# Kernel optimization log

Measured on AMD Instinct MI355X. Metric: run time of the kernel, lower is better.

Reference implementation:

```python
import jax, jax.numpy as jnp
import numpy as np

D = 1024      # input_dim
H = 1024      # expert_hidden_dim
O = 1024      # output_dim
E = 8         # num_experts
TOPK = 2
B, N_OBJ = 4, 4096


def setup_inputs() -> dict:
    key = jax.random.key(0)
    ks = jax.random.split(key, 7)
    s_in = 1.0 / np.sqrt(D)
    s_h = 1.0 / np.sqrt(H)
    return {
        "x":  jax.random.normal(ks[0], (B, N_OBJ, D), dtype=jnp.float32),
        "Wr": jax.random.uniform(ks[1], (D, E), jnp.float32, -s_in, s_in),
        "br": jax.random.uniform(ks[2], (E,), jnp.float32, -s_in, s_in),
        "W1": jax.random.uniform(ks[3], (E, D, H), jnp.float32, -s_in, s_in),
        "b1": jax.random.uniform(ks[4], (E, H), jnp.float32, -s_in, s_in),
        "W2": jax.random.uniform(ks[5], (E, H, O), jnp.float32, -s_h, s_h),
        "b2": jax.random.uniform(ks[6], (E, O), jnp.float32, -s_h, s_h),
    }


def reference(x, Wr, br, W1, b1, W2, b2):
    # Router: (B, N, E)
    logits = jnp.einsum("bnd,de->bne", x, Wr) + br
    # sparse top-k routing: softmax over the top-k logits only
    topv, topi = jax.lax.top_k(logits, TOPK)          # (B, N, k)
    coef = jax.nn.softmax(topv, axis=-1)              # (B, N, k)
    # scatter per-expert coefficients into dense (B, N, E); zeros for non-selected
    coef_full = jnp.sum(
        jax.nn.one_hot(topi, E, dtype=x.dtype) * coef[..., None], axis=-2
    )                                                 # (B, N, E)
    # All-expert dense compute (as in original module; dropout is eval-mode identity)
    h = jax.nn.relu(jnp.einsum("bnd,edh->benh", x, W1) + b1[:, None, :])  # (B,E,N,H)
    y = jnp.einsum("benh,eho->beno", h, W2) + b2[:, None, :]              # (B,E,N,O)
    # Weighted combine over experts
    out = jnp.einsum("beno,bne->bno", y, coef_full)                        # (B,N,O)
    return out
```

## Files before the change

### kernel.cpp

```cpp
#include <hip/hip_runtime.h>
#include <cstdint>

typedef unsigned short u16;
using bf16x8 = __attribute__((ext_vector_type(8))) __bf16;
using f32x4  = __attribute__((ext_vector_type(4))) float;

#define T_TOK 16384
#define E_NUM 8

__device__ __forceinline__ u16 f2bf(float f) {
    union { float f; unsigned u; } v; v.f = f;
    unsigned r = (v.u + 0x7FFFu + ((v.u >> 16) & 1u)) >> 16;
    return (u16)r;
}

__device__ __forceinline__ void gload_lds16(const void* g, void* l) {
    __builtin_amdgcn_global_load_lds(
        (const __attribute__((address_space(1))) void*)g,
        (__attribute__((address_space(3))) void*)l, 16, 0, 0);
}

__global__ __launch_bounds__(256) void k_transpose(const float* __restrict__ W, u16* __restrict__ WT) {
    __shared__ float tile[32][33];
    int e = blockIdx.z;
    int d0 = blockIdx.x << 5, h0 = blockIdx.y << 5;
    int tx = threadIdx.x & 31, ty = threadIdx.x >> 5;
    const size_t eo = (size_t)e << 20;
#pragma unroll
    for (int i = 0; i < 4; ++i) {
        int r = ty + i * 8;
        tile[r][tx] = W[eo + (size_t)(d0 + r) * 1024 + h0 + tx];
    }
    __syncthreads();
#pragma unroll
    for (int i = 0; i < 4; ++i) {
        int r = ty + i * 8;
        WT[eo + (size_t)(h0 + r) * 1024 + d0 + tx] = f2bf(tile[tx][r]);
    }
}

__global__ __launch_bounds__(256) void k_router(const float* __restrict__ x, const float* __restrict__ Wr,
                                                const float* __restrict__ br,
                                                int* __restrict__ tinfo, float* __restrict__ c1arr,
                                                u16* __restrict__ xbf) {
    const int wave = threadIdx.x >> 6, lane = threadIdx.x & 63;
    const int t = (blockIdx.x << 2) + wave;
    const float* xr = x + (size_t)t * 1024;
    u16* xbr = xbf + (size_t)t * 1024;
    float acc[8] = {0, 0, 0, 0, 0, 0, 0, 0};
#pragma unroll
    for (int i = 0; i < 16; ++i) {
        int d = (i << 6) + lane;
        float xv = xr[d];
        xbr[d] = f2bf(xv);
        float4 w0 = *(const float4*)(Wr + d * 8);
        float4 w1 = *(const float4*)(Wr + d * 8 + 4);
        acc[0] += xv * w0.x; acc[1] += xv * w0.y; acc[2] += xv * w0.z; acc[3] += xv * w0.w;
        acc[4] += xv * w1.x; acc[5] += xv * w1.y; acc[6] += xv * w1.z; acc[7] += xv * w1.w;
    }
#pragma unroll
    for (int off = 32; off > 0; off >>= 1)
#pragma unroll
        for (int e = 0; e < 8; ++e) acc[e] += __shfl_xor(acc[e], off);

    if (lane == 0) {
        float v1 = -1e30f, v2 = -1e30f; int i1 = 0, i2 = 0;
#pragma unroll
        for (int e = 0; e < 8; ++e) {
            float v = acc[e] + br[e];
            if (v > v1) { v2 = v1; i2 = i1; v1 = v; i1 = e; }
            else if (v > v2) { v2 = v; i2 = e; }
        }
        float c1 = 1.f / (1.f + expf(v2 - v1));
        tinfo[t] = i1 | (i2 << 4);
        c1arr[t] = c1;
    }
}

__global__ __launch_bounds__(1024) void k_scatter(const int* __restrict__ tinfo, const float* __restrict__ c1arr,
                                                  int* __restrict__ cnt, int* __restrict__ tok,
                                                  float* __restrict__ coef) {
    __shared__ int lcnt[8];
    __shared__ int lbase[8];
    const int tid = threadIdx.x;
    const int t = blockIdx.x * 1024 + tid;
    if (tid < 8) lcnt[tid] = 0;
    __syncthreads();
    int info = tinfo[t];
    float c1 = c1arr[t];
    int g1 = info & 15;
    int g2 = (info >> 4) & 15;
    int o1 = atomicAdd(&lcnt[g1], 1);
    int o2 = atomicAdd(&lcnt[g2], 1);
    __syncthreads();
    if (tid < 8) lbase[tid] = atomicAdd(cnt + tid, lcnt[tid]);
    __syncthreads();
    int p1 = lbase[g1] + o1;
    tok[(g1 << 14) + p1] = t; coef[(g1 << 14) + p1] = c1;
    int p2 = lbase[g2] + o2;
    tok[(g2 << 14) + p2] = t; coef[(g2 << 14) + p2] = 1.f - c1;
}

template <int PHASE>
__global__ __launch_bounds__(256, 3) void k_gemm(
    const int* __restrict__ cnt, const int* __restrict__ tok, const float* __restrict__ coef,
    const u16* __restrict__ xbf, const u16* __restrict__ w1t, const u16* __restrict__ w2t,
    const float* __restrict__ b1, const float* __restrict__ b2,
    u16* __restrict__ hbuf, float* __restrict__ out)
{
    __shared__ u16 a0_s[128 * 64];
    __shared__ u16 a1_s[128 * 64];
    __shared__ u16 b0_s[64 * 64];
    __shared__ u16 b1_s[64 * 64];
    __shared__ int s_cnt[8];
    __shared__ int tok_s[128];
    __shared__ float coef_s[128];

    const int tid = threadIdx.x;
    if (tid < 8) s_cnt[tid] = cnt[tid];
    __syncthreads();

    int bid = blockIdx.x + blockIdx.y * 272;
    int lin = (bid & 7) * 544 + (bid >> 3);
    int xt = lin >> 4, yt = lin & 15;

    int g = -1, tile = 0, r0 = 0, mt = xt, rb = 0;
    for (int gg = 0; gg < 8; ++gg) {
        int c = s_cnt[gg], tg = (c + 127) >> 7;
        if (g < 0) {
            if (mt < tg) { g = gg; tile = mt; r0 = rb + (mt << 7); }
            else mt -= tg;
        }
        rb += c;
    }
    if (g < 0) return;
    const int cntg = s_cnt[g];
    const int e = g;
    const int nb = yt << 6;
    const int rowlim = cntg - (tile << 7);

    if (tid < 128) {
        int idx = (tile << 7) + tid;
        bool valid = idx < cntg;
        tok_s[tid] = valid ? tok[(g << 14) + idx] : 0;
        coef_s[tid] = valid ? coef[(g << 14) + idx] : 0.f;
    }
    __syncthreads();

    const int w = tid >> 6, l = tid & 63;
    const int wrow = (w >> 1) << 6, wcol = (w & 1) << 5;
    const u16* asrc = (PHASE == 0) ? xbf : hbuf;
    const u16* bsrc = (PHASE == 0) ? w1t : w2t;
    const size_t brow0 = ((size_t)e << 10) + nb;

    const int sw = ((l & 7) ^ (l >> 3)) << 3;
    const int xk = (l & 7) << 3;

    const u16* aptr[4]; int ldsa[4];
#pragma unroll
    for (int j = 0; j < 4; ++j) {
        int row = (j << 5) + (w << 3) + (l >> 3);
        int arow = (PHASE == 0) ? tok_s[row] : (r0 + row);
        aptr[j] = asrc + ((size_t)arow << 10) + sw;
        ldsa[j] = ((j << 5) + (w << 3)) * 64;
    }
    const u16* bptr[2]; int ldsb[2];
#pragma unroll
    for (int j = 0; j < 2; ++j) {
        int brow = (j << 5) + (w << 3) + (l >> 3);
        bptr[j] = bsrc + (brow0 + brow) * 1024 + sw;
        ldsb[j] = ((j << 5) + (w << 3)) * 64;
    }

    f32x4 acc[4][2];
#pragma unroll
    for (int mi = 0; mi < 4; ++mi)
#pragma unroll
        for (int ni = 0; ni < 2; ++ni) { acc[mi][ni][0] = 0.f; acc[mi][ni][1] = 0.f; acc[mi][ni][2] = 0.f; acc[mi][ni][3] = 0.f; }

#define STAGE(AS, BS, KO)                                                      \
    {                                                                          \
        _Pragma("unroll")                                                      \
        for (int j = 0; j < 4; ++j) gload_lds16(aptr[j] + (KO), &AS[ldsa[j]]); \
        _Pragma("unroll")                                                      \
        for (int j = 0; j < 2; ++j) gload_lds16(bptr[j] + (KO), &BS[ldsb[j]]); \
    }

#define COMPUTE(AS, BS)                                                        \
    {                                                                          \
        _Pragma("unroll")                                                      \
        for (int ks = 0; ks < 64; ks += 32) {                                  \
            const int co = (ks + ((l >> 4) << 3)) ^ xk;                        \
            bf16x8 af[4], bfr[2];                                              \
            _Pragma("unroll")                                                  \
            for (int mi = 0; mi < 4; ++mi)                                     \
                af[mi] = *(const bf16x8*)&AS[(wrow + (mi << 4) + (l & 15)) * 64 + co]; \
            _Pragma("unroll")                                                  \
            for (int ni = 0; ni < 2; ++ni)                                     \
                bfr[ni] = *(const bf16x8*)&BS[(wcol + (ni << 4) + (l & 15)) * 64 + co]; \
            _Pragma("unroll")                                                  \
            for (int mi = 0; mi < 4; ++mi)                                     \
                _Pragma("unroll")                                              \
                for (int ni = 0; ni < 2; ++ni)                                 \
                    acc[mi][ni] = __builtin_amdgcn_mfma_f32_16x16x32_bf16(af[mi], bfr[ni], acc[mi][ni], 0, 0, 0); \
        }                                                                      \
    }

#define VM6  asm volatile("s_waitcnt vmcnt(6)" ::: "memory")
#define VM0  asm volatile("s_waitcnt vmcnt(0)" ::: "memory")
#define LGK0 asm volatile("s_waitcnt lgkmcnt(0)" ::: "memory")
#define BAR() { asm volatile("" ::: "memory"); __builtin_amdgcn_s_barrier(); asm volatile("" ::: "memory"); }

    STAGE(a0_s, b0_s, 0);
    STAGE(a1_s, b1_s, 64);
    VM6; BAR();

    for (int kc = 0; kc < 12; kc += 2) {
        COMPUTE(a0_s, b0_s);
        LGK0; BAR();
        STAGE(a0_s, b0_s, (kc + 2) << 6);
        VM6; BAR();
        COMPUTE(a1_s, b1_s);
        LGK0; BAR();
        STAGE(a1_s, b1_s, (kc + 3) << 6);
        VM6; BAR();
    }
    COMPUTE(a0_s, b0_s);
    LGK0; BAR();
    STAGE(a0_s, b0_s, 14 << 6);
    VM6; BAR();
    COMPUTE(a1_s, b1_s);
    LGK0; BAR();
    STAGE(a1_s, b1_s, 15 << 6);
    VM6; BAR();
    COMPUTE(a0_s, b0_s);
    LGK0; BAR();
    VM0; BAR();
    COMPUTE(a1_s, b1_s);

#undef STAGE
#undef COMPUTE
#undef VM6
#undef VM0
#undef LGK0
#undef BAR

    const int rq = (l >> 4) << 2;
    const int cl = l & 15;
#pragma unroll
    for (int ni = 0; ni < 2; ++ni) {
        int ccol = wcol + (ni << 4) + cl;
        float bias = (PHASE == 0 ? b1 : b2)[((size_t)e << 10) + nb + ccol];
#pragma unroll
        for (int mi = 0; mi < 4; ++mi) {
            int rbase = wrow + (mi << 4) + rq;
#pragma unroll
            for (int j = 0; j < 4; ++j) {
                int r = rbase + j;
                if (r < rowlim) {
                    float v = acc[mi][ni][j] + bias;
                    if constexpr (PHASE == 0) {
                        v = fmaxf(v, 0.f);
                        hbuf[(size_t)(r0 + r) * 1024 + nb + ccol] = f2bf(v);
                    } else {
                        atomicAdd(out + ((size_t)tok_s[r] << 10) + nb + ccol, v * coef_s[r]);
                    }
                }
            }
        }
    }
}

__global__ __launch_bounds__(256) void k_naive(const float* __restrict__ x, const float* __restrict__ Wr,
    const float* __restrict__ br, const float* __restrict__ W1, const float* __restrict__ b1,
    const float* __restrict__ W2, const float* __restrict__ b2, float* __restrict__ out)
{
    __shared__ float xs[1024];
    __shared__ float hs[1024];
    __shared__ float red[4];
    __shared__ float lg[8];
    const int tid = threadIdx.x;
    const size_t t = blockIdx.x;
    for (int i = tid; i < 1024; i += 256) xs[i] = x[t * 1024 + i];
    __syncthreads();
    float lacc[8] = {0, 0, 0, 0, 0, 0, 0, 0};
    for (int d = tid; d < 1024; d += 256) {
        float xv = xs[d];
#pragma unroll
        for (int e = 0; e < 8; ++e) lacc[e] += xv * Wr[d * 8 + e];
    }
    for (int e = 0; e < 8; ++e) {
        float v = lacc[e];
        for (int off = 32; off > 0; off >>= 1) v += __shfl_xor(v, off);
        if ((tid & 63) == 0) red[tid >> 6] = v;
        __syncthreads();
        if (tid == 0) lg[e] = red[0] + red[1] + red[2] + red[3] + br[e];
        __syncthreads();
    }
    float v1 = -1e30f, v2 = -1e30f; int i1 = 0, i2 = 0;
    for (int e = 0; e < 8; ++e) {
        float v = lg[e];
        if (v > v1) { v2 = v1; i2 = i1; v1 = v; i1 = e; }
        else if (v > v2) { v2 = v; i2 = e; }
    }
    float c1 = 1.f / (1.f + expf(v2 - v1)), c2 = 1.f - c1;
    float yacc[4] = {0, 0, 0, 0};
    for (int slot = 0; slot < 2; ++slot) {
        int e = slot ? i2 : i1;
        float cw = slot ? c2 : c1;
        __syncthreads();
        float ha[4];
        for (int jb = 0; jb < 4; ++jb) {
            int j = (jb << 8) + tid;
            float a = b1[(e << 10) + j];
            for (int d = 0; d < 1024; ++d) a += xs[d] * W1[(((size_t)e << 10) + d) * 1024 + j];
            ha[jb] = fmaxf(a, 0.f);
        }
        for (int jb = 0; jb < 4; ++jb) hs[(jb << 8) + tid] = ha[jb];
        __syncthreads();
        for (int ob = 0; ob < 4; ++ob) {
            int o = (ob << 8) + tid;
            float a = b2[(e << 10) + o];
            for (int h = 0; h < 1024; ++h) a += hs[h] * W2[(((size_t)e << 10) + h) * 1024 + o];
            yacc[ob] += cw * a;
        }
    }
    for (int ob = 0; ob < 4; ++ob) out[t * 1024 + (ob << 8) + tid] = yacc[ob];
}

extern "C" void kernel_launch(void* const* d_in, const int* in_sizes, int n_in,
                              void* d_out, int out_size, void* d_ws, size_t ws_size,
                              hipStream_t stream) {
    const float* x  = (const float*)d_in[0];
    const float* Wr = (const float*)d_in[1];
    const float* br = (const float*)d_in[2];
    const float* W1 = (const float*)d_in[3];
    const float* b1 = (const float*)d_in[4];
    const float* W2 = (const float*)d_in[5];
    const float* b2 = (const float*)d_in[6];
    float* out = (float*)d_out;

    const size_t OFF_TOK   = (size_t)1 << 20;
    const size_t OFF_COEF  = (size_t)2 << 20;
    const size_t OFF_TINFO = (size_t)3 << 20;
    const size_t OFF_C1    = OFF_TINFO + (size_t)T_TOK * 4;
    const size_t OFF_XBF   = (size_t)4 << 20;
    const size_t OFF_W1T   = OFF_XBF + (size_t)T_TOK * 1024 * 2;
    const size_t OFF_W2T   = OFF_W1T + (size_t)E_NUM * 1024 * 1024 * 2;
    const size_t OFF_H     = OFF_W2T + (size_t)E_NUM * 1024 * 1024 * 2;
    const size_t WS_NEED   = OFF_H + (size_t)(2 * T_TOK + 512) * 1024 * 2;

    if (ws_size < WS_NEED) {
        k_naive<<<T_TOK, 256, 0, stream>>>(x, Wr, br, W1, b1, W2, b2, out);
        return;
    }

    char* ws = (char*)d_ws;
    int*   cnt   = (int*)ws;
    int*   tok   = (int*)(ws + OFF_TOK);
    float* coef  = (float*)(ws + OFF_COEF);
    int*   tinfo = (int*)(ws + OFF_TINFO);
    float* c1arr = (float*)(ws + OFF_C1);
    u16*   xbf   = (u16*)(ws + OFF_XBF);
    u16*   w1t   = (u16*)(ws + OFF_W1T);
    u16*   w2t   = (u16*)(ws + OFF_W2T);
    u16*   hbuf  = (u16*)(ws + OFF_H);

    hipMemsetAsync(cnt, 0, 64, stream);
    hipMemsetAsync(d_out, 0, (size_t)out_size * sizeof(float), stream);
    k_transpose<<<dim3(32, 32, 8), 256, 0, stream>>>(W1, w1t);
    k_transpose<<<dim3(32, 32, 8), 256, 0, stream>>>(W2, w2t);
    k_router<<<4096, 256, 0, stream>>>(x, Wr, br, tinfo, c1arr, xbf);
    k_scatter<<<16, 1024, 0, stream>>>(tinfo, c1arr, cnt, tok, coef);
    dim3 gg(272, 16);
    k_gemm<0><<<gg, 256, 0, stream>>>(cnt, tok, coef, xbf, w1t, w2t, b1, b2, hbuf, out);
    k_gemm<1><<<gg, 256, 0, stream>>>(cnt, tok, coef, xbf, w1t, w2t, b1, b2, hbuf, out);
}
```

Before: 393.1 us.

## Single-buffer B tile and drop shared token tables to fit four blocks per CU

```diff
diff --git a/kernel.cpp b/kernel.cpp
--- a/kernel.cpp
+++ b/kernel.cpp
@@ -102,7 +102,7 @@
 }
 
 template <int PHASE>
-__global__ __launch_bounds__(256, 3) void k_gemm(
+__global__ __launch_bounds__(256, 4) void k_gemm(
     const int* __restrict__ cnt, const int* __restrict__ tok, const float* __restrict__ coef,
     const u16* __restrict__ xbf, const u16* __restrict__ w1t, const u16* __restrict__ w2t,
     const float* __restrict__ b1, const float* __restrict__ b2,
@@ -110,23 +110,17 @@
 {
     __shared__ u16 a0_s[128 * 64];
     __shared__ u16 a1_s[128 * 64];
-    __shared__ u16 b0_s[64 * 64];
-    __shared__ u16 b1_s[64 * 64];
-    __shared__ int s_cnt[8];
-    __shared__ int tok_s[128];
-    __shared__ float coef_s[128];
-
+    __shared__ u16 b_s[64 * 64];
     const int tid = threadIdx.x;
-    if (tid < 8) s_cnt[tid] = cnt[tid];
-    __syncthreads();
 
     int bid = blockIdx.x + blockIdx.y * 272;
     int lin = (bid & 7) * 544 + (bid >> 3);
     int xt = lin >> 4, yt = lin & 15;
 
     int g = -1, tile = 0, r0 = 0, mt = xt, rb = 0;
+#pragma unroll
     for (int gg = 0; gg < 8; ++gg) {
-        int c = s_cnt[gg], tg = (c + 127) >> 7;
+        int c = cnt[gg], tg = (c + 127) >> 7;
         if (g < 0) {
             if (mt < tg) { g = gg; tile = mt; r0 = rb + (mt << 7); }
             else mt -= tg;
@@ -134,18 +128,11 @@
         rb += c;
     }
     if (g < 0) return;
-    const int cntg = s_cnt[g];
+    const int cntg = cnt[g];
     const int e = g;
     const int nb = yt << 6;
     const int rowlim = cntg - (tile << 7);
-
-    if (tid < 128) {
-        int idx = (tile << 7) + tid;
-        bool valid = idx < cntg;
-        tok_s[tid] = valid ? tok[(g << 14) + idx] : 0;
-        coef_s[tid] = valid ? coef[(g << 14) + idx] : 0.f;
-    }
-    __syncthreads();
+    const int gbase = (g << 14) + (tile << 7);
 
     const int w = tid >> 6, l = tid & 63;
     const int wrow = (w >> 1) << 6, wcol = (w & 1) << 5;
@@ -160,7 +147,13 @@
 #pragma unroll
     for (int j = 0; j < 4; ++j) {
         int row = (j << 5) + (w << 3) + (l >> 3);
-        int arow = (PHASE == 0) ? tok_s[row] : (r0 + row);
+        int arow;
+        if (PHASE == 0) {
+            int idx = gbase + row;
+            arow = (row < rowlim) ? tok[idx] : 0;
+        } else {
+            arow = r0 + row;
+        }
         aptr[j] = asrc + ((size_t)arow << 10) + sw;
         ldsa[j] = ((j << 5) + (w << 3)) * 64;
     }
@@ -178,15 +171,18 @@
 #pragma unroll
         for (int ni = 0; ni < 2; ++ni) { acc[mi][ni][0] = 0.f; acc[mi][ni][1] = 0.f; acc[mi][ni][2] = 0.f; acc[mi][ni][3] = 0.f; }
 
-#define STAGE(AS, BS, KO)                                                      \
+#define STAGE_A(AS, KO)                                                        \
     {                                                                          \
         _Pragma("unroll")                                                      \
         for (int j = 0; j < 4; ++j) gload_lds16(aptr[j] + (KO), &AS[ldsa[j]]); \
+    }
+#define STAGE_B(KO)                                                            \
+    {                                                                          \
         _Pragma("unroll")                                                      \
-        for (int j = 0; j < 2; ++j) gload_lds16(bptr[j] + (KO), &BS[ldsb[j]]); \
-    }
-
-#define COMPUTE(AS, BS)                                                        \
+        for (int j = 0; j < 2; ++j) gload_lds16(bptr[j] + (KO), &b_s[ldsb[j]]); \
+    }
+
+#define COMPUTE(AS)                                                            \
     {                                                                          \
         _Pragma("unroll")                                                      \
         for (int ks = 0; ks < 64; ks += 32) {                                  \
@@ -197,7 +193,7 @@
                 af[mi] = *(const bf16x8*)&AS[(wrow + (mi << 4) + (l & 15)) * 64 + co]; \
             _Pragma("unroll")                                                  \
             for (int ni = 0; ni < 2; ++ni)                                     \
-                bfr[ni] = *(const bf16x8*)&BS[(wcol + (ni << 4) + (l & 15)) * 64 + co]; \
+                bfr[ni] = *(const bf16x8*)&b_s[(wcol + (ni << 4) + (l & 15)) * 64 + co]; \
             _Pragma("unroll")                                                  \
             for (int mi = 0; mi < 4; ++mi)                                     \
                 _Pragma("unroll")                                              \
@@ -206,41 +202,38 @@
         }                                                                      \
     }
 
-#define VM6  asm volatile("s_waitcnt vmcnt(6)" ::: "memory")
+#define VM4  asm volatile("s_waitcnt vmcnt(4)" ::: "memory")
 #define VM0  asm volatile("s_waitcnt vmcnt(0)" ::: "memory")
 #define LGK0 asm volatile("s_waitcnt lgkmcnt(0)" ::: "memory")
 #define BAR() { asm volatile("" ::: "memory"); __builtin_amdgcn_s_barrier(); asm volatile("" ::: "memory"); }
 
-    STAGE(a0_s, b0_s, 0);
-    STAGE(a1_s, b1_s, 64);
-    VM6; BAR();
-
-    for (int kc = 0; kc < 12; kc += 2) {
-        COMPUTE(a0_s, b0_s);
+    STAGE_A(a0_s, 0);
+    STAGE_B(0);
+    STAGE_A(a1_s, 64);
+    VM4; BAR();
+
+    for (int kc = 0; kc < 14; kc += 2) {
+        COMPUTE(a0_s);
         LGK0; BAR();
-        STAGE(a0_s, b0_s, (kc + 2) << 6);
-        VM6; BAR();
-        COMPUTE(a1_s, b1_s);
+        STAGE_B((kc + 1) << 6);
+        STAGE_A(a0_s, (kc + 2) << 6);
+        VM4; BAR();
+        COMPUTE(a1_s);
         LGK0; BAR();
-        STAGE(a1_s, b1_s, (kc + 3) << 6);
-        VM6; BAR();
-    }
-    COMPUTE(a0_s, b0_s);
+        STAGE_B((kc + 2) << 6);
+        STAGE_A(a1_s, (kc + 3) << 6);
+        VM4; BAR();
+    }
+    COMPUTE(a0_s);
     LGK0; BAR();
-    STAGE(a0_s, b0_s, 14 << 6);
-    VM6; BAR();
-    COMPUTE(a1_s, b1_s);
-    LGK0; BAR();
-    STAGE(a1_s, b1_s, 15 << 6);
-    VM6; BAR();
-    COMPUTE(a0_s, b0_s);
-    LGK0; BAR();
+    STAGE_B(15 << 6);
     VM0; BAR();
-    COMPUTE(a1_s, b1_s);
-
-#undef STAGE
+    COMPUTE(a1_s);
+
+#undef STAGE_A
+#undef STAGE_B
 #undef COMPUTE
-#undef VM6
+#undef VM4
 #undef VM0
 #undef LGK0
 #undef BAR
@@ -263,7 +256,8 @@
                         v = fmaxf(v, 0.f);
                         hbuf[(size_t)(r0 + r) * 1024 + nb + ccol] = f2bf(v);
                     } else {
-                        atomicAdd(out + ((size_t)tok_s[r] << 10) + nb + ccol, v * coef_s[r]);
+                        int gi = gbase + r;
+                        atomicAdd(out + ((size_t)tok[gi] << 10) + nb + ccol, v * coef[gi]);
                     }
                 }
             }
```

Measured after the change: 376.4 us. -4.3%, faster.
